# Kernel tuning notes

Measured on AMD Instinct MI355X. Metric: run time of the kernel, lower is better.

Reference implementation:

```python
import jax, jax.numpy as jnp
import numpy as np
import math

QUERY_DIM = 1024
KEY_DIM = 768
VALUE_DIM = 768
NUM_HEADS = 16
HEAD_DIM = QUERY_DIM // NUM_HEADS


def setup_inputs() -> dict:
    key = jax.random.key(0)
    ks = jax.random.split(key, 11)
    B, Sq, Skv = 4, 2048, 2048
    query = jax.random.normal(ks[0], (B, Sq, QUERY_DIM), dtype=jnp.float32)
    k_in = jax.random.normal(ks[1], (B, Skv, KEY_DIM), dtype=jnp.float32)
    v_in = jax.random.normal(ks[2], (B, Skv, VALUE_DIM), dtype=jnp.float32)
    # Linear weights stored as [in, out] (y = x @ W + b), equivalent to torch's x @ W^T.
    def lin(k, fan_in, fan_out):
        bound = 1.0 / math.sqrt(fan_in)
        kw, kb = jax.random.split(k)
        W = jax.random.uniform(kw, (fan_in, fan_out), minval=-bound, maxval=bound, dtype=jnp.float32)
        b = jax.random.uniform(kb, (fan_out,), minval=-bound, maxval=bound, dtype=jnp.float32)
        return W, b
    Wq, bq = lin(ks[3], QUERY_DIM, QUERY_DIM)
    Wk, bk = lin(ks[4], KEY_DIM, QUERY_DIM)
    Wv, bv = lin(ks[5], VALUE_DIM, QUERY_DIM)
    Wo, bo = lin(ks[6], QUERY_DIM, QUERY_DIM)
    return {"query": query, "key": k_in, "value": v_in,
            "Wq": Wq, "bq": bq, "Wk": Wk, "bk": bk,
            "Wv": Wv, "bv": bv, "Wo": Wo, "bo": bo}


def reference(query, key, value, Wq, bq, Wk, bk, Wv, bv, Wo, bo):
    B, Sq, _ = query.shape
    H, D = NUM_HEADS, HEAD_DIM
    # Projections -> [B, H, S, D]
    Q = (query @ Wq + bq).reshape(B, Sq, H, D).transpose(0, 2, 1, 3)
    K = (key @ Wk + bk).reshape(B, -1, H, D).transpose(0, 2, 1, 3)
    V = (value @ Wv + bv).reshape(B, -1, H, D).transpose(0, 2, 1, 3)
    scale = 1.0 / math.sqrt(D)
    scores = jnp.einsum('bhqd,bhkd->bhqk', Q, K) * scale  # [B,H,Sq,Skv]
    weights = jax.nn.softmax(scores, axis=-1)
    attended = jnp.einsum('bhqk,bhkd->bhqd', weights, V)
    attended = attended.transpose(0, 2, 1, 3).reshape(B, Sq, H * D)
    # torch .squeeze(1): no-op since Sq > 1
    return attended @ Wo + bo
```

## Files before the change

kernel.cpp:

```cpp
#include <hip/hip_runtime.h>

#define B_ 4
#define SQ 2048
#define SKV 2048
#define DMODEL 1024
#define DKV 768
#define NH 16
#define DH 64

typedef unsigned short u16;
typedef __bf16 bf16x4 __attribute__((ext_vector_type(4)));
typedef __bf16 bf16x8 __attribute__((ext_vector_type(8)));
typedef float f32x4 __attribute__((ext_vector_type(4)));
typedef float f32x16 __attribute__((ext_vector_type(16)));

__device__ __forceinline__ u16 f2bf(float f) {
  union { __bf16 b; u16 u; } cv;
  cv.b = (__bf16)f;
  return cv.u;
}

__device__ __forceinline__ unsigned cvtpk(float lo, float hi) {
  unsigned r;
  asm("v_cvt_pk_bf16_f32 %0, %1, %2" : "=v"(r) : "v"(lo), "v"(hi));
  return r;
}

__device__ __forceinline__ float fexp2(float x) {
  float r;
  asm("v_exp_f32 %0, %1" : "=v"(r) : "v"(x));
  return r;
}

#define GLDS(gp, lp) __builtin_amdgcn_global_load_lds(                         \
    (const __attribute__((address_space(1))) unsigned*)(gp),                   \
    (__attribute__((address_space(3))) unsigned*)(lp), 16, 0, 0)

__global__ __launch_bounds__(256)
void wt4_kernel(const float* __restrict__ W0, const float* __restrict__ W1,
                const float* __restrict__ W2, const float* __restrict__ W3,
                u16* __restrict__ T0, u16* __restrict__ T1,
                u16* __restrict__ T2, u16* __restrict__ T3) {
  const int z = blockIdx.z;
  const float* W = (z == 0) ? W0 : (z == 1) ? W1 : (z == 2) ? W2 : W3;
  u16* T = (z == 0) ? T0 : (z == 1) ? T1 : (z == 2) ? T2 : T3;
  const int K = (z == 1 || z == 2) ? DKV : DMODEL;
  const int N = DMODEL;
  int n0 = blockIdx.x * 32, k0 = blockIdx.y * 32;
  if (k0 >= K) return;
  __shared__ float tl[32][33];
  int tx = threadIdx.x, ty = threadIdx.y;
#pragma unroll
  for (int p = 0; p < 4; ++p)
    tl[ty + 8 * p][tx] = W[(size_t)(k0 + ty + 8 * p) * N + n0 + tx];
  __syncthreads();
#pragma unroll
  for (int p = 0; p < 4; ++p)
    T[(size_t)(n0 + ty + 8 * p) * K + k0 + tx] = f2bf(tl[tx][ty + 8 * p]);
}

__global__ __launch_bounds__(256)
void qkv_kernel(const float* __restrict__ Aq, const float* __restrict__ Ak,
                const float* __restrict__ Av,
                const u16* __restrict__ Wtq, const u16* __restrict__ Wtk,
                const u16* __restrict__ Wtv,
                const float* __restrict__ bq, const float* __restrict__ bk,
                const float* __restrict__ bv,
                float sclq,
                u16* __restrict__ Qp, u16* __restrict__ Kp, u16* __restrict__ Vt) {
  __shared__ __align__(16) u16 Alds[128][88];
  __shared__ __align__(16) u16 Blds[128][64];
  const int z = blockIdx.z;
  const float* Af = (z == 0) ? Aq : (z == 1) ? Ak : Av;
  const u16* Wt = (z == 0) ? Wtq : (z == 1) ? Wtk : Wtv;
  const float* bias = (z == 0) ? bq : (z == 1) ? bk : bv;
  const int K = (z == 0) ? DMODEL : DKV;
  const float oscale = (z == 0) ? sclq : 1.0f;

  const int t = threadIdx.x;
  const int l = t & 63;
  const int lx = l & 15, lg = l >> 4;
  const int wid = t >> 6;
  const int wr = wid >> 1, wc = wid & 1;

  int flat = blockIdx.y * 8 + blockIdx.x;
  int by = (flat & 7) * 8 + ((flat >> 3) & 7);
  int bx = flat >> 6;
  const int m0 = by * 128, n0 = bx * 128;

  const int srow = l >> 3;
  const int scol = (l & 7) * 8;

  f32x4 acc[4][4];
#pragma unroll
  for (int i = 0; i < 4; ++i)
#pragma unroll
    for (int j = 0; j < 4; ++j) acc[i][j] = (f32x4){0.f, 0.f, 0.f, 0.f};

  const int arow = t >> 4;
  const int acol = (t & 15) * 4;
  const float* abase = Af + (size_t)(m0 + arow) * K + acol;

  float4 areg[8];
#pragma unroll
  for (int p = 0; p < 8; ++p)
    areg[p] = *(const float4*)(abase + (size_t)p * 16 * K);

  for (int k0 = 0; k0 < K; k0 += 64) {
    __syncthreads();
#pragma unroll
    for (int j = 0; j < 4; ++j) {
      int row = wid * 32 + j * 8;
      GLDS(Wt + (size_t)(n0 + row + srow) * K + k0 + scol, &Blds[row][0]);
    }
#pragma unroll
    for (int p = 0; p < 8; ++p) {
      union { bf16x4 v; uint2 u; } cv;
      cv.v[0] = (__bf16)areg[p].x; cv.v[1] = (__bf16)areg[p].y;
      cv.v[2] = (__bf16)areg[p].z; cv.v[3] = (__bf16)areg[p].w;
      *(uint2*)(&Alds[p * 16 + arow][acol]) = cv.u;
    }
    __syncthreads();
    if ((k0 + 64) < K) {
#pragma unroll
      for (int p = 0; p < 8; ++p)
        areg[p] = *(const float4*)(abase + (size_t)p * 16 * K + k0 + 64);
    }
#pragma unroll
    for (int kk = 0; kk < 64; kk += 32) {
      bf16x8 af[4], bfr[4];
#pragma unroll
      for (int i = 0; i < 4; ++i)
        af[i] = *(const bf16x8*)(&Alds[wr * 64 + i * 16 + lx][kk + lg * 8]);
#pragma unroll
      for (int j = 0; j < 4; ++j)
        bfr[j] = *(const bf16x8*)(&Blds[wc * 64 + j * 16 + lx][kk + lg * 8]);
#pragma unroll
      for (int i = 0; i < 4; ++i)
#pragma unroll
        for (int j = 0; j < 4; ++j)
          acc[i][j] = __builtin_amdgcn_mfma_f32_16x16x32_bf16(af[i], bfr[j], acc[i][j], 0, 0, 0);
    }
  }
#pragma unroll
  for (int j = 0; j < 4; ++j) {
    int col = n0 + wc * 64 + j * 16 + lx;
    float bv = bias[col];
#pragma unroll
    for (int i = 0; i < 4; ++i) {
      int rowb = m0 + wr * 64 + i * 16 + lg * 4;
      f32x4 c = acc[i][j];
      if (z == 2) {
        int b = rowb >> 11, s = rowb & 2047;
        int h = col >> 6, d = col & 63;
        u16* vt = Vt + (size_t)((b * NH + h) * DH + d) * SKV + s;
        union { bf16x4 v; uint2 u; } cv;
        cv.v[0] = (__bf16)(c[0] + bv); cv.v[1] = (__bf16)(c[1] + bv);
        cv.v[2] = (__bf16)(c[2] + bv); cv.v[3] = (__bf16)(c[3] + bv);
        *(uint2*)vt = cv.u;
      } else {
        u16* op = (z == 0) ? Qp : Kp;
#pragma unroll
        for (int r = 0; r < 4; ++r)
          op[(size_t)(rowb + r) * DMODEL + col] = f2bf((c[r] + bv) * oscale);
      }
    }
  }
}

__global__ __launch_bounds__(256)
void oproj_kernel(const u16* __restrict__ Ab, const u16* __restrict__ Wt,
                  const float* __restrict__ bias, float* __restrict__ out_) {
  const int M = B_ * SQ, N = DMODEL, K = DMODEL;
  __shared__ __align__(16) u16 Alds[128][64];
  __shared__ __align__(16) u16 Blds[128][64];
  const int t = threadIdx.x;
  const int l = t & 63;
  const int lx = l & 15, lg = l >> 4;
  const int wid = t >> 6;
  const int wr = wid >> 1, wc = wid & 1;

  int flat = blockIdx.y * 8 + blockIdx.x;
  int by = (flat & 7) * 8 + ((flat >> 3) & 7);
  int bx = flat >> 6;
  const int m0 = by * 128, n0 = bx * 128;

  const int srow = l >> 3;
  const int scol = (l & 7) * 8;

  f32x4 acc[4][4];
#pragma unroll
  for (int i = 0; i < 4; ++i)
#pragma unroll
    for (int j = 0; j < 4; ++j) acc[i][j] = (f32x4){0.f, 0.f, 0.f, 0.f};

  for (int k0 = 0; k0 < K; k0 += 64) {
    __syncthreads();
#pragma unroll
    for (int j = 0; j < 4; ++j) {
      int row = wid * 32 + j * 8;
      GLDS(Wt + (size_t)(n0 + row + srow) * K + k0 + scol, &Blds[row][0]);
      GLDS(Ab + (size_t)(m0 + row + srow) * K + k0 + scol, &Alds[row][0]);
    }
    __syncthreads();
#pragma unroll
    for (int kk = 0; kk < 64; kk += 32) {
      bf16x8 af[4], bfr[4];
#pragma unroll
      for (int i = 0; i < 4; ++i)
        af[i] = *(const bf16x8*)(&Alds[wr * 64 + i * 16 + lx][kk + lg * 8]);
#pragma unroll
      for (int j = 0; j < 4; ++j)
        bfr[j] = *(const bf16x8*)(&Blds[wc * 64 + j * 16 + lx][kk + lg * 8]);
#pragma unroll
      for (int i = 0; i < 4; ++i)
#pragma unroll
        for (int j = 0; j < 4; ++j)
          acc[i][j] = __builtin_amdgcn_mfma_f32_16x16x32_bf16(af[i], bfr[j], acc[i][j], 0, 0, 0);
    }
  }
#pragma unroll
  for (int j = 0; j < 4; ++j) {
    int col = n0 + wc * 64 + j * 16 + lx;
    float bv = bias[col];
#pragma unroll
    for (int i = 0; i < 4; ++i) {
      int rowb = m0 + wr * 64 + i * 16 + lg * 4;
      f32x4 c = acc[i][j];
#pragma unroll
      for (int r = 0; r < 4; ++r)
        out_[(size_t)(rowb + r) * N + col] = c[r] + bv;
    }
  }
}

#define KVB 64
#define KP 72

__global__ __launch_bounds__(256)
void attn_kernel(const u16* __restrict__ Qp, const u16* __restrict__ Kp,
                 const u16* __restrict__ Vt, u16* __restrict__ Att) {
  __shared__ __align__(16) u16 Klds[2][KVB][KP];
  __shared__ __align__(16) u16 Vlds[2][DH][KP];
  const int t = threadIdx.x;
  const int l = t & 63;
  const int ql = l & 31, hi = l >> 5;
  const int wid = t >> 6;

  const int flat = blockIdx.y * 16 + blockIdx.x;
  const int xcd = flat & 7;
  const int rest = flat >> 3;
  const int bh = xcd * 8 + (rest & 7);
  const int qb = rest >> 3;
  const int b = bh >> 4, h = bh & 15;
  const int q = qb * 128 + wid * 32 + ql;

  bf16x8 qf[4];
  const u16* qbase = Qp + (size_t)(b * SQ + q) * DMODEL + h * 64 + hi * 8;
#pragma unroll
  for (int ds = 0; ds < 4; ++ds) qf[ds] = *(const bf16x8*)(qbase + ds * 16);

  bf16x8 ones;
  {
    union { unsigned u[4]; bf16x8 v; } o;
    o.u[0] = o.u[1] = o.u[2] = o.u[3] = 0x3F803F80u;
    ones = o.v;
  }
  f32x16 z16;
#pragma unroll
  for (int r = 0; r < 16; ++r) z16[r] = 0.f;

  f32x16 acc0, acc1, sacc;
#pragma unroll
  for (int r = 0; r < 16; ++r) { acc0[r] = 0.f; acc1[r] = 0.f; sacc[r] = 0.f; }

  const int sr = t >> 2;
  const int sc = (t & 3) * 16;
  const u16* kg = Kp + (size_t)(b * SKV) * DMODEL + h * 64;
  const u16* vg = Vt + ((size_t)(b * NH + h) * DH + sr) * SKV;

  {
    const u16* kp_ = kg + (size_t)sr * DMODEL + sc;
    uint4 k0 = *(const uint4*)kp_, k1 = *(const uint4*)(kp_ + 8);
    uint4 v0 = *(const uint4*)(vg + sc), v1 = *(const uint4*)(vg + sc + 8);
    *(uint4*)(&Klds[0][sr][sc]) = k0; *(uint4*)(&Klds[0][sr][sc + 8]) = k1;
    *(uint4*)(&Vlds[0][sr][sc]) = v0; *(uint4*)(&Vlds[0][sr][sc + 8]) = v1;
  }
  int cur = 0;
  const int h0 = wid & 1;

  for (int kv0 = 0; kv0 < SKV; kv0 += KVB) {
    uint4 kr0, kr1, vr0, vr1;
    const bool pf = (kv0 + KVB) < SKV;
    if (pf) {
      const u16* kp_ = kg + (size_t)(kv0 + KVB + sr) * DMODEL + sc;
      kr0 = *(const uint4*)kp_; kr1 = *(const uint4*)(kp_ + 8);
      const u16* vp_ = vg + kv0 + KVB + sc;
      vr0 = *(const uint4*)vp_; vr1 = *(const uint4*)(vp_ + 8);
    }
    __syncthreads();

#pragma unroll
    for (int ph = 0; ph < 2; ++ph) {
      const int hf = ph ^ h0;
      const int krow = hf * 32 + ql;
      f32x16 st;
      __builtin_amdgcn_s_setprio(1);
      {
        bf16x8 k0 = *(const bf16x8*)(&Klds[cur][krow][hi * 8]);
        st = __builtin_amdgcn_mfma_f32_32x32x16_bf16(k0, qf[0], z16, 0, 0, 0);
      }
#pragma unroll
      for (int ds = 1; ds < 4; ++ds) {
        bf16x8 kk = *(const bf16x8*)(&Klds[cur][krow][ds * 16 + hi * 8]);
        st = __builtin_amdgcn_mfma_f32_32x32x16_bf16(kk, qf[ds], st, 0, 0, 0);
      }
      __builtin_amdgcn_s_setprio(0);

#pragma unroll
      for (int r = 0; r < 16; ++r) st[r] = fexp2(st[r]);

      unsigned pk[8];
#pragma unroll
      for (int j = 0; j < 8; ++j) pk[j] = cvtpk(st[2 * j], st[2 * j + 1]);

      __builtin_amdgcn_s_setprio(1);
#pragma unroll
      for (int ksl = 0; ksl < 2; ++ksl) {
        auto wA = __builtin_amdgcn_permlane32_swap(pk[4 * ksl + 0], pk[4 * ksl + 2], false, false);
        auto wB = __builtin_amdgcn_permlane32_swap(pk[4 * ksl + 1], pk[4 * ksl + 3], false, false);
        union { unsigned w[4]; bf16x8 v; } pfr;
        pfr.w[0] = (unsigned)wA[0]; pfr.w[1] = (unsigned)wB[0];
        pfr.w[2] = (unsigned)wA[1]; pfr.w[3] = (unsigned)wB[1];
        int ks = hf * 2 + ksl;
        bf16x8 v0 = *(const bf16x8*)(&Vlds[cur][ql][ks * 16 + hi * 8]);
        bf16x8 v1 = *(const bf16x8*)(&Vlds[cur][32 + ql][ks * 16 + hi * 8]);
        acc0 = __builtin_amdgcn_mfma_f32_32x32x16_bf16(v0, pfr.v, acc0, 0, 0, 0);
        acc1 = __builtin_amdgcn_mfma_f32_32x32x16_bf16(v1, pfr.v, acc1, 0, 0, 0);
        sacc = __builtin_amdgcn_mfma_f32_32x32x16_bf16(ones, pfr.v, sacc, 0, 0, 0);
      }
      __builtin_amdgcn_s_setprio(0);
    }

    if (pf) {
      int nxt = cur ^ 1;
      *(uint4*)(&Klds[nxt][sr][sc]) = kr0; *(uint4*)(&Klds[nxt][sr][sc + 8]) = kr1;
      *(uint4*)(&Vlds[nxt][sr][sc]) = vr0; *(uint4*)(&Vlds[nxt][sr][sc + 8]) = vr1;
    }
    cur ^= 1;
  }

  float inv = 1.0f / sacc[0];
  u16* ob = Att + (size_t)(b * SQ + q) * DMODEL + h * 64;
#pragma unroll
  for (int dt = 0; dt < 2; ++dt) {
    const f32x16& a = dt ? acc1 : acc0;
#pragma unroll
    for (int g = 0; g < 4; ++g) {
      unsigned w0 = cvtpk(a[4 * g] * inv, a[4 * g + 1] * inv);
      unsigned w1 = cvtpk(a[4 * g + 2] * inv, a[4 * g + 3] * inv);
      *(uint2*)(ob + dt * 32 + g * 8 + hi * 4) = make_uint2(w0, w1);
    }
  }
}

extern "C" void kernel_launch(void* const* d_in, const int* in_sizes, int n_in,
                              void* d_out, int out_size, void* d_ws, size_t ws_size,
                              hipStream_t stream) {
  const float* query = (const float*)d_in[0];
  const float* key   = (const float*)d_in[1];
  const float* value = (const float*)d_in[2];
  const float* Wq = (const float*)d_in[3];
  const float* bq = (const float*)d_in[4];
  const float* Wk = (const float*)d_in[5];
  const float* bk = (const float*)d_in[6];
  const float* Wv = (const float*)d_in[7];
  const float* bv = (const float*)d_in[8];
  const float* Wo = (const float*)d_in[9];
  const float* bo = (const float*)d_in[10];
  float* out = (float*)d_out;

  u16* ws = (u16*)d_ws;
  const size_t MTOK = (size_t)B_ * SQ;
  u16* Qp  = ws;
  u16* Kp  = Qp + MTOK * DMODEL;
  u16* Vtb = Kp + MTOK * DMODEL;
  u16* Att = Vtb + MTOK * DMODEL;
  u16* WqT = Att + MTOK * DMODEL;
  u16* WkT = WqT + (size_t)DMODEL * DMODEL;
  u16* WvT = WkT + (size_t)DKV * DMODEL;
  u16* WoT = WvT + (size_t)DKV * DMODEL;

  const float SCL = 0.18033688011112042f;

  dim3 tb(32, 8);
  wt4_kernel<<<dim3(DMODEL / 32, DMODEL / 32, 4), tb, 0, stream>>>(
      Wq, Wk, Wv, Wo, WqT, WkT, WvT, WoT);

  qkv_kernel<<<dim3(DMODEL / 128, MTOK / 128, 3), 256, 0, stream>>>(
      query, key, value, WqT, WkT, WvT, bq, bk, bv, SCL, Qp, Kp, Vtb);

  attn_kernel<<<dim3(SQ / 128, B_ * NH), 256, 0, stream>>>(Qp, Kp, Vtb, Att);

  oproj_kernel<<<dim3(DMODEL / 128, MTOK / 128), 256, 0, stream>>>(Att, WoT, bo, out);
}
```

Before: 204.0 us.

## Double attention block to 512 threads and process both KV halves per wave

The attention kernel now uses 8 waves per block covering 256 queries, so each K/V tile staged in LDS serves twice as many queries. Each thread loads half as much per tile. Each wave now computes both 32-row KV halves' scores together (two independent MFMA chains) instead of two sequential phases, which adds instruction-level parallelism. The cost is higher register pressure from two live score tiles, half as many blocks (512), and a bigger barrier group.

```diff
diff --git a/kernel.cpp b/kernel.cpp
--- a/kernel.cpp
+++ b/kernel.cpp
@@ -171,7 +171,7 @@
 __global__ __launch_bounds__(256)
 void oproj_kernel(const u16* __restrict__ Ab, const u16* __restrict__ Wt,
                   const float* __restrict__ bias, float* __restrict__ out_) {
-  const int M = B_ * SQ, N = DMODEL, K = DMODEL;
+  const int N = DMODEL, K = DMODEL;
   __shared__ __align__(16) u16 Alds[128][64];
   __shared__ __align__(16) u16 Blds[128][64];
   const int t = threadIdx.x;
@@ -237,7 +237,7 @@
 #define KVB 64
 #define KP 72
 
-__global__ __launch_bounds__(256)
+__global__ __launch_bounds__(512)
 void attn_kernel(const u16* __restrict__ Qp, const u16* __restrict__ Kp,
                  const u16* __restrict__ Vt, u16* __restrict__ Att) {
   __shared__ __align__(16) u16 Klds[2][KVB][KP];
@@ -247,13 +247,13 @@
   const int ql = l & 31, hi = l >> 5;
   const int wid = t >> 6;
 
-  const int flat = blockIdx.y * 16 + blockIdx.x;
+  const int flat = blockIdx.y * 8 + blockIdx.x;
   const int xcd = flat & 7;
   const int rest = flat >> 3;
   const int bh = xcd * 8 + (rest & 7);
   const int qb = rest >> 3;
   const int b = bh >> 4, h = bh & 15;
-  const int q = qb * 128 + wid * 32 + ql;
+  const int q = qb * 256 + wid * 32 + ql;
 
   bf16x8 qf[4];
   const u16* qbase = Qp + (size_t)(b * SQ + q) * DMODEL + h * 64 + hi * 8;
@@ -274,57 +274,55 @@
 #pragma unroll
   for (int r = 0; r < 16; ++r) { acc0[r] = 0.f; acc1[r] = 0.f; sacc[r] = 0.f; }
 
-  const int sr = t >> 2;
-  const int sc = (t & 3) * 16;
+  const int sr = t >> 3;
+  const int sc = (t & 7) * 8;
   const u16* kg = Kp + (size_t)(b * SKV) * DMODEL + h * 64;
   const u16* vg = Vt + ((size_t)(b * NH + h) * DH + sr) * SKV;
 
   {
-    const u16* kp_ = kg + (size_t)sr * DMODEL + sc;
-    uint4 k0 = *(const uint4*)kp_, k1 = *(const uint4*)(kp_ + 8);
-    uint4 v0 = *(const uint4*)(vg + sc), v1 = *(const uint4*)(vg + sc + 8);
-    *(uint4*)(&Klds[0][sr][sc]) = k0; *(uint4*)(&Klds[0][sr][sc + 8]) = k1;
-    *(uint4*)(&Vlds[0][sr][sc]) = v0; *(uint4*)(&Vlds[0][sr][sc + 8]) = v1;
+    uint4 k0 = *(const uint4*)(kg + (size_t)sr * DMODEL + sc);
+    uint4 v0 = *(const uint4*)(vg + sc);
+    *(uint4*)(&Klds[0][sr][sc]) = k0;
+    *(uint4*)(&Vlds[0][sr][sc]) = v0;
   }
   int cur = 0;
-  const int h0 = wid & 1;
 
   for (int kv0 = 0; kv0 < SKV; kv0 += KVB) {
-    uint4 kr0, kr1, vr0, vr1;
+    uint4 kr0, vr0;
     const bool pf = (kv0 + KVB) < SKV;
     if (pf) {
-      const u16* kp_ = kg + (size_t)(kv0 + KVB + sr) * DMODEL + sc;
-      kr0 = *(const uint4*)kp_; kr1 = *(const uint4*)(kp_ + 8);
-      const u16* vp_ = vg + kv0 + KVB + sc;
-      vr0 = *(const uint4*)vp_; vr1 = *(const uint4*)(vp_ + 8);
+      kr0 = *(const uint4*)(kg + (size_t)(kv0 + KVB + sr) * DMODEL + sc);
+      vr0 = *(const uint4*)(vg + kv0 + KVB + sc);
     }
     __syncthreads();
 
-#pragma unroll
-    for (int ph = 0; ph < 2; ++ph) {
-      const int hf = ph ^ h0;
-      const int krow = hf * 32 + ql;
-      f32x16 st;
-      __builtin_amdgcn_s_setprio(1);
-      {
-        bf16x8 k0 = *(const bf16x8*)(&Klds[cur][krow][hi * 8]);
-        st = __builtin_amdgcn_mfma_f32_32x32x16_bf16(k0, qf[0], z16, 0, 0, 0);
-      }
-#pragma unroll
-      for (int ds = 1; ds < 4; ++ds) {
-        bf16x8 kk = *(const bf16x8*)(&Klds[cur][krow][ds * 16 + hi * 8]);
-        st = __builtin_amdgcn_mfma_f32_32x32x16_bf16(kk, qf[ds], st, 0, 0, 0);
-      }
-      __builtin_amdgcn_s_setprio(0);
-
-#pragma unroll
-      for (int r = 0; r < 16; ++r) st[r] = fexp2(st[r]);
-
+    f32x16 st0, st1;
+    __builtin_amdgcn_s_setprio(1);
+    {
+      bf16x8 k0 = *(const bf16x8*)(&Klds[cur][ql][hi * 8]);
+      bf16x8 k1 = *(const bf16x8*)(&Klds[cur][32 + ql][hi * 8]);
+      st0 = __builtin_amdgcn_mfma_f32_32x32x16_bf16(k0, qf[0], z16, 0, 0, 0);
+      st1 = __builtin_amdgcn_mfma_f32_32x32x16_bf16(k1, qf[0], z16, 0, 0, 0);
+    }
+#pragma unroll
+    for (int ds = 1; ds < 4; ++ds) {
+      bf16x8 k0 = *(const bf16x8*)(&Klds[cur][ql][ds * 16 + hi * 8]);
+      bf16x8 k1 = *(const bf16x8*)(&Klds[cur][32 + ql][ds * 16 + hi * 8]);
+      st0 = __builtin_amdgcn_mfma_f32_32x32x16_bf16(k0, qf[ds], st0, 0, 0, 0);
+      st1 = __builtin_amdgcn_mfma_f32_32x32x16_bf16(k1, qf[ds], st1, 0, 0, 0);
+    }
+    __builtin_amdgcn_s_setprio(0);
+
+#pragma unroll
+    for (int r = 0; r < 16; ++r) { st0[r] = fexp2(st0[r]); st1[r] = fexp2(st1[r]); }
+
+    __builtin_amdgcn_s_setprio(1);
+#pragma unroll
+    for (int tt = 0; tt < 2; ++tt) {
+      const f32x16& stt = tt ? st1 : st0;
       unsigned pk[8];
 #pragma unroll
-      for (int j = 0; j < 8; ++j) pk[j] = cvtpk(st[2 * j], st[2 * j + 1]);
-
-      __builtin_amdgcn_s_setprio(1);
+      for (int j = 0; j < 8; ++j) pk[j] = cvtpk(stt[2 * j], stt[2 * j + 1]);
 #pragma unroll
       for (int ksl = 0; ksl < 2; ++ksl) {
         auto wA = __builtin_amdgcn_permlane32_swap(pk[4 * ksl + 0], pk[4 * ksl + 2], false, false);
@@ -332,20 +330,20 @@
         union { unsigned w[4]; bf16x8 v; } pfr;
         pfr.w[0] = (unsigned)wA[0]; pfr.w[1] = (unsigned)wB[0];
         pfr.w[2] = (unsigned)wA[1]; pfr.w[3] = (unsigned)wB[1];
-        int ks = hf * 2 + ksl;
+        int ks = tt * 2 + ksl;
         bf16x8 v0 = *(const bf16x8*)(&Vlds[cur][ql][ks * 16 + hi * 8]);
         bf16x8 v1 = *(const bf16x8*)(&Vlds[cur][32 + ql][ks * 16 + hi * 8]);
         acc0 = __builtin_amdgcn_mfma_f32_32x32x16_bf16(v0, pfr.v, acc0, 0, 0, 0);
         acc1 = __builtin_amdgcn_mfma_f32_32x32x16_bf16(v1, pfr.v, acc1, 0, 0, 0);
         sacc = __builtin_amdgcn_mfma_f32_32x32x16_bf16(ones, pfr.v, sacc, 0, 0, 0);
       }
-      __builtin_amdgcn_s_setprio(0);
-    }
+    }
+    __builtin_amdgcn_s_setprio(0);
 
     if (pf) {
       int nxt = cur ^ 1;
-      *(uint4*)(&Klds[nxt][sr][sc]) = kr0; *(uint4*)(&Klds[nxt][sr][sc + 8]) = kr1;
-      *(uint4*)(&Vlds[nxt][sr][sc]) = vr0; *(uint4*)(&Vlds[nxt][sr][sc + 8]) = vr1;
+      *(uint4*)(&Klds[nxt][sr][sc]) = kr0;
+      *(uint4*)(&Vlds[nxt][sr][sc]) = vr0;
     }
     cur ^= 1;
   }
@@ -400,7 +398,7 @@
   qkv_kernel<<<dim3(DMODEL / 128, MTOK / 128, 3), 256, 0, stream>>>(
       query, key, value, WqT, WkT, WvT, bq, bk, bv, SCL, Qp, Kp, Vtb);
 
-  attn_kernel<<<dim3(SQ / 128, B_ * NH), 256, 0, stream>>>(Qp, Kp, Vtb, Att);
+  attn_kernel<<<dim3(SQ / 256, B_ * NH), 512, 0, stream>>>(Qp, Kp, Vtb, Att);
 
   oproj_kernel<<<dim3(DMODEL / 128, MTOK / 128), 256, 0, stream>>>(Att, WoT, bo, out);
 }
```

Result: faster. 184.8 us (-9.4%).
